# Kernel optimization log

Measured on AMD Instinct MI355X. Metric: run time of the kernel, lower is better.

## Reference

```python
import jax, jax.numpy as jnp
import numpy as np

B, IN, OUT = 131072, 256, 256
BITWIDTH = 7.0


def setup_inputs() -> dict:
    key = jax.random.key(0)
    k1, k2 = jax.random.split(key)
    # simulated int8 activations (integer-valued float32)
    act_in = jax.random.randint(k1, (B, IN), -127, 128).astype(jnp.float32)
    # UniformWeights: xavier_uniform then weight_quant to the int8 grid
    limit = float(np.sqrt(6.0 / (IN + OUT)))
    w = jax.random.uniform(k2, (OUT, IN), minval=-limit, maxval=limit, dtype=jnp.float32)
    w_range = jnp.max(jnp.abs(w))
    weight_exp = (jnp.ceil(jnp.log2(w_range)) - 7.0).astype(jnp.int32)
    weight = jnp.round(w / w_range * 127.0)  # int8-valued float32 [OUT, IN]
    return {"act_in": act_in, "exp_in": jnp.int32(0), "weight": weight, "weight_exp": weight_exp}


def _round_shift(x, shift):
    # RoundShift: floor-div by 2**shift, add floor(|remainder| / 2**(shift-1)), clip to int8
    two_s = jnp.exp2(shift)
    rt = jnp.floor(x / two_s)
    prob = jnp.abs(x - rt * two_s)
    dec = jnp.floor(prob / jnp.exp2(shift - 1.0))
    return jnp.clip(rt + dec, -127.0, 127.0)


def reference(act_in, exp_in, weight, weight_exp):
    # int8 GEMM simulated in fp32 (exact: |acc| < 2^24)
    temp = act_in @ weight.T  # [B, OUT] int32 accumulator values
    # RangeEstimate: full-tensor abs-max -> bitwidth
    r = jnp.max(jnp.abs(temp))
    bw = jnp.where(r > 0, jnp.ceil(jnp.log2(jnp.maximum(r, 1.0))), 0.0)
    shift = bw - BITWIDTH
    pos = shift > 0
    safe_shift = jnp.maximum(shift, 1.0)
    rounded = _round_shift(temp, safe_shift)
    act_out = jnp.where(pos, rounded, temp).astype(jnp.int8)
    exp_sum = jnp.asarray(exp_in, jnp.int32) + jnp.asarray(weight_exp, jnp.int32)
    exp_out = (exp_sum + jnp.where(pos, shift, 0.0).astype(jnp.int32)).astype(jnp.int16)
    return act_out, exp_out
```

## Files before the change

### kernel.cpp

```cpp
#include <hip/hip_runtime.h>
#include <stdint.h>


#define M_ROWS 131072
#define NK 256
#define BM 64
#define BK 64
#define BKP 72

typedef __attribute__((ext_vector_type(8))) short bf16x8;
typedef __attribute__((ext_vector_type(4))) float f32x4;
typedef __attribute__((ext_vector_type(4))) float fv4;
typedef __attribute__((ext_vector_type(4))) int iv4;
typedef __attribute__((ext_vector_type(4))) unsigned int u32x4;
typedef __attribute__((ext_vector_type(4))) unsigned short us4;

__device__ __forceinline__ uint32_t pack_bf16(float a, float b) {
  return (__float_as_uint(a) >> 16) | (__float_as_uint(b) & 0xFFFF0000u);
}

__global__ void wconv(const float* __restrict__ w, unsigned short* __restrict__ wb) {
  const int i = blockIdx.x * 256 + threadIdx.x;
  const fv4 f = ((const fv4*)w)[i];
  us4 o;
  o.x = (unsigned short)(__float_as_uint(f.x) >> 16);
  o.y = (unsigned short)(__float_as_uint(f.y) >> 16);
  o.z = (unsigned short)(__float_as_uint(f.z) >> 16);
  o.w = (unsigned short)(__float_as_uint(f.w) >> 16);
  ((us4*)wb)[i] = o;
}

__device__ __forceinline__ void gemm_tile(
    const float* __restrict__ act, const unsigned short* __restrict__ wgtb,
    short* As, short* Bs, f32x4 acc[4][4])
{
  const int tid  = threadIdx.x;
  const int bm   = blockIdx.x * BM;
  const int lane = tid & 63;
  const int wave = tid >> 6;
  const int lm   = lane & 15;
  const int lk   = lane >> 4;
  const int wn   = wave * 64;

  const int arow = tid >> 3, aks = (tid & 7) * 8;
  const int brow = tid >> 3, bks = (tid & 7) * 8;

  uint32_t apk[2][4];
  u32x4 breg[8];

#pragma unroll
  for (int j = 0; j < 2; ++j) {
    const float* p = act + (size_t)(bm + arow + j * 32) * NK + aks;
    const fv4 f0 = *(const fv4*)p;
    const fv4 f1 = *((const fv4*)p + 1);
    apk[j][0] = pack_bf16(f0.x, f0.y); apk[j][1] = pack_bf16(f0.z, f0.w);
    apk[j][2] = pack_bf16(f1.x, f1.y); apk[j][3] = pack_bf16(f1.z, f1.w);
  }
#pragma unroll
  for (int j = 0; j < 8; ++j)
    breg[j] = *(const u32x4*)(wgtb + (size_t)(brow + j * 32) * NK + bks);

  for (int kt = 0; kt < NK; kt += BK) {
    __syncthreads();
#pragma unroll
    for (int j = 0; j < 2; ++j)
      *(u32x4*)&As[(arow + j * 32) * BKP + aks] = *(const u32x4*)apk[j];
#pragma unroll
    for (int j = 0; j < 8; ++j)
      *(u32x4*)&Bs[(brow + j * 32) * BKP + bks] = breg[j];
    __syncthreads();

    if (kt + BK < NK) {
      const int ktn = kt + BK;
#pragma unroll
      for (int j = 0; j < 2; ++j) {
        const float* p = act + (size_t)(bm + arow + j * 32) * NK + ktn + aks;
        const fv4 f0 = *(const fv4*)p;
        const fv4 f1 = *((const fv4*)p + 1);
        apk[j][0] = pack_bf16(f0.x, f0.y); apk[j][1] = pack_bf16(f0.z, f0.w);
        apk[j][2] = pack_bf16(f1.x, f1.y); apk[j][3] = pack_bf16(f1.z, f1.w);
      }
#pragma unroll
      for (int j = 0; j < 8; ++j)
        breg[j] = *(const u32x4*)(wgtb + (size_t)(brow + j * 32) * NK + ktn + bks);
    }

#pragma unroll
    for (int kk = 0; kk < BK; kk += 32) {
      bf16x8 af[4], bfr[4];
#pragma unroll
      for (int mi = 0; mi < 4; ++mi)
        af[mi] = *(const bf16x8*)&As[(mi * 16 + lm) * BKP + kk + lk * 8];
#pragma unroll
      for (int ni = 0; ni < 4; ++ni)
        bfr[ni] = *(const bf16x8*)&Bs[(wn + ni * 16 + lm) * BKP + kk + lk * 8];
#pragma unroll
      for (int mi = 0; mi < 4; ++mi)
#pragma unroll
        for (int ni = 0; ni < 4; ++ni)
          acc[mi][ni] = __builtin_amdgcn_mfma_f32_16x16x32_bf16(
              af[mi], bfr[ni], acc[mi][ni], 0, 0, 0);
    }
  }
}

__global__ __launch_bounds__(256, 3) void gemm_max(
    const float* __restrict__ act, const unsigned short* __restrict__ wgtb,
    int* __restrict__ gmax)
{
  __shared__ __align__(16) short As[BM * BKP];
  __shared__ __align__(16) short Bs[NK * BKP];
  __shared__ int smax;
  const int tid = threadIdx.x;
  if (tid == 0) smax = 0;

  f32x4 acc[4][4] = {};
  gemm_tile(act, wgtb, As, Bs, acc);

  int imax = 0;
#pragma unroll
  for (int mi = 0; mi < 4; ++mi)
#pragma unroll
    for (int ni = 0; ni < 4; ++ni)
#pragma unroll
      for (int r = 0; r < 4; ++r) {
        const int iv = (int)acc[mi][ni][r];
        const int a = iv < 0 ? -iv : iv;
        imax = a > imax ? a : imax;
      }
#pragma unroll
  for (int off = 32; off; off >>= 1) {
    const int o = __shfl_xor(imax, off, 64);
    imax = o > imax ? o : imax;
  }
  if ((tid & 63) == 0) atomicMax(&smax, imax);
  __syncthreads();
  if (tid == 0) atomicMax(gmax, smax);
}

__global__ __launch_bounds__(256, 3) void gemm_quant(
    const float* __restrict__ act, const unsigned short* __restrict__ wgtb,
    int* __restrict__ out, const int* __restrict__ gmax,
    const int* __restrict__ exp_in, const int* __restrict__ wexp)
{
  __shared__ __align__(16) short As[BM * BKP];
  __shared__ __align__(16) short Bs[NK * BKP];

  const int rmax = *gmax;
  const int bw = (rmax <= 1) ? 0 : (32 - __clz(rmax - 1));
  const int shift = bw - 7;
  const bool pos = shift > 0;
  const int s = shift < 1 ? 1 : shift;

  f32x4 acc[4][4] = {};
  gemm_tile(act, wgtb, As, Bs, acc);

  const int tid  = threadIdx.x;
  const int bm   = blockIdx.x * BM;
  const int lane = tid & 63;
  const int lm   = lane & 15;
  const int lk   = lane >> 4;
  const int wn   = (tid >> 6) * 64;

#pragma unroll
  for (int mi = 0; mi < 4; ++mi)
#pragma unroll
    for (int ni = 0; ni < 4; ++ni)
#pragma unroll
      for (int r = 0; r < 4; ++r) {
        const int ti = (int)acc[mi][ni][r];
        int q;
        if (pos) {
          const int rt = ti >> s;
          const int dec = (ti - (rt << s)) >> (s - 1);
          q = rt + dec;
          q = q > 127 ? 127 : (q < -127 ? -127 : q);
        } else {
          q = (int)(signed char)(ti & 0xFF);
        }
        const int m = bm + mi * 16 + lk * 4 + r;
        const int n = wn + ni * 16 + lm;
        __builtin_nontemporal_store(q, &out[(size_t)m * NK + n]);
      }

  if (blockIdx.x == 0 && tid == 0) {
    const int e = exp_in[0] + wexp[0] + (pos ? shift : 0);
    out[(size_t)M_ROWS * NK] = (int)(short)e;
  }
}

extern "C" void kernel_launch(void* const* d_in, const int* in_sizes, int n_in,
                              void* d_out, int out_size, void* d_ws, size_t ws_size,
                              hipStream_t stream) {
  const float* act   = (const float*)d_in[0];
  const int* exp_in  = (const int*)d_in[1];
  const float* wgt   = (const float*)d_in[2];
  const int* wexp    = (const int*)d_in[3];
  int* gmax          = (int*)d_ws;
  unsigned short* wb = (unsigned short*)((char*)d_ws + 128);

  (void)hipMemsetAsync(d_ws, 0, sizeof(int), stream);
  wconv<<<dim3(64), dim3(256), 0, stream>>>(wgt, wb);
  gemm_max<<<dim3(M_ROWS / BM), dim3(256), 0, stream>>>(act, wb, gmax);
  gemm_quant<<<dim3(M_ROWS / BM), dim3(256), 0, stream>>>(act, wb, (int*)d_out,
                                                          gmax, exp_in, wexp);
}
```

Baseline: 280.2 us.

## Store raw accumulators in first GEMM pass and requantize in place

Instead of running the GEMM twice (once for the global max, once for quantization), the first pass writes int32 accumulators to the output buffer. A lightweight elementwise pass then requantizes them in place. The memset is folded into the weight conversion kernel. This avoids recomputing the GEMM and rereading activations, at the cost of an extra write and read of the 128MB output buffer.

```diff
diff --git a/kernel.cpp b/kernel.cpp
--- a/kernel.cpp
+++ b/kernel.cpp
@@ -19,7 +19,9 @@
   return (__float_as_uint(a) >> 16) | (__float_as_uint(b) & 0xFFFF0000u);
 }
 
-__global__ void wconv(const float* __restrict__ w, unsigned short* __restrict__ wb) {
+__global__ void wconv(const float* __restrict__ w, unsigned short* __restrict__ wb,
+                      int* __restrict__ gmax) {
+  if (blockIdx.x == 0 && threadIdx.x == 0) *gmax = 0;
   const int i = blockIdx.x * 256 + threadIdx.x;
   const fv4 f = ((const fv4*)w)[i];
   us4 o;
@@ -104,9 +106,9 @@
   }
 }
 
-__global__ __launch_bounds__(256, 3) void gemm_max(
+__global__ __launch_bounds__(256, 3) void gemm_maxstore(
     const float* __restrict__ act, const unsigned short* __restrict__ wgtb,
-    int* __restrict__ gmax)
+    int* __restrict__ out, int* __restrict__ gmax)
 {
   __shared__ __align__(16) short As[BM * BKP];
   __shared__ __align__(16) short Bs[NK * BKP];
@@ -117,6 +119,12 @@
   f32x4 acc[4][4] = {};
   gemm_tile(act, wgtb, As, Bs, acc);
 
+  const int bm   = blockIdx.x * BM;
+  const int lane = tid & 63;
+  const int lm   = lane & 15;
+  const int lk   = lane >> 4;
+  const int wn   = (tid >> 6) * 64;
+
   int imax = 0;
 #pragma unroll
   for (int mi = 0; mi < 4; ++mi)
@@ -124,9 +132,12 @@
     for (int ni = 0; ni < 4; ++ni)
 #pragma unroll
       for (int r = 0; r < 4; ++r) {
-        const int iv = (int)acc[mi][ni][r];
-        const int a = iv < 0 ? -iv : iv;
+        const int ti = (int)acc[mi][ni][r];
+        const int a = ti < 0 ? -ti : ti;
         imax = a > imax ? a : imax;
+        const int m = bm + mi * 16 + lk * 4 + r;
+        const int n = wn + ni * 16 + lm;
+        out[(size_t)m * NK + n] = ti;
       }
 #pragma unroll
   for (int off = 32; off; off >>= 1) {
@@ -138,52 +149,40 @@
   if (tid == 0) atomicMax(gmax, smax);
 }
 
-__global__ __launch_bounds__(256, 3) void gemm_quant(
-    const float* __restrict__ act, const unsigned short* __restrict__ wgtb,
+__global__ __launch_bounds__(256) void quant_pass(
     int* __restrict__ out, const int* __restrict__ gmax,
     const int* __restrict__ exp_in, const int* __restrict__ wexp)
 {
-  __shared__ __align__(16) short As[BM * BKP];
-  __shared__ __align__(16) short Bs[NK * BKP];
-
   const int rmax = *gmax;
   const int bw = (rmax <= 1) ? 0 : (32 - __clz(rmax - 1));
   const int shift = bw - 7;
   const bool pos = shift > 0;
   const int s = shift < 1 ? 1 : shift;
 
-  f32x4 acc[4][4] = {};
-  gemm_tile(act, wgtb, As, Bs, acc);
-
-  const int tid  = threadIdx.x;
-  const int bm   = blockIdx.x * BM;
-  const int lane = tid & 63;
-  const int lm   = lane & 15;
-  const int lk   = lane >> 4;
-  const int wn   = (tid >> 6) * 64;
-
-#pragma unroll
-  for (int mi = 0; mi < 4; ++mi)
-#pragma unroll
-    for (int ni = 0; ni < 4; ++ni)
-#pragma unroll
-      for (int r = 0; r < 4; ++r) {
-        const int ti = (int)acc[mi][ni][r];
-        int q;
-        if (pos) {
-          const int rt = ti >> s;
-          const int dec = (ti - (rt << s)) >> (s - 1);
-          q = rt + dec;
-          q = q > 127 ? 127 : (q < -127 ? -127 : q);
-        } else {
-          q = (int)(signed char)(ti & 0xFF);
-        }
-        const int m = bm + mi * 16 + lk * 4 + r;
-        const int n = wn + ni * 16 + lm;
-        __builtin_nontemporal_store(q, &out[(size_t)m * NK + n]);
+  const size_t total  = (size_t)M_ROWS * NK / 4;
+  const size_t stride = (size_t)gridDim.x * blockDim.x;
+  for (size_t i = (size_t)blockIdx.x * blockDim.x + threadIdx.x; i < total;
+       i += stride) {
+    iv4 t = ((const iv4*)out)[i];
+    iv4 q;
+#pragma unroll
+    for (int j = 0; j < 4; ++j) {
+      const int ti = t[j];
+      int r;
+      if (pos) {
+        const int rt = ti >> s;
+        const int dec = (ti - (rt << s)) >> (s - 1);
+        r = rt + dec;
+        r = r > 127 ? 127 : (r < -127 ? -127 : r);
+      } else {
+        r = (int)(signed char)(ti & 0xFF);
       }
-
-  if (blockIdx.x == 0 && tid == 0) {
+      q[j] = r;
+    }
+    __builtin_nontemporal_store(q, &((iv4*)out)[i]);
+  }
+
+  if (blockIdx.x == 0 && threadIdx.x == 0) {
     const int e = exp_in[0] + wexp[0] + (pos ? shift : 0);
     out[(size_t)M_ROWS * NK] = (int)(short)e;
   }
@@ -199,9 +198,8 @@
   int* gmax          = (int*)d_ws;
   unsigned short* wb = (unsigned short*)((char*)d_ws + 128);
 
-  (void)hipMemsetAsync(d_ws, 0, sizeof(int), stream);
-  wconv<<<dim3(64), dim3(256), 0, stream>>>(wgt, wb);
-  gemm_max<<<dim3(M_ROWS / BM), dim3(256), 0, stream>>>(act, wb, gmax);
-  gemm_quant<<<dim3(M_ROWS / BM), dim3(256), 0, stream>>>(act, wb, (int*)d_out,
-                                                          gmax, exp_in, wexp);
-}
+  wconv<<<dim3(64), dim3(256), 0, stream>>>(wgt, wb, gmax);
+  gemm_maxstore<<<dim3(M_ROWS / BM), dim3(256), 0, stream>>>(act, wb, (int*)d_out,
+                                                             gmax);
+  quant_pass<<<dim3(2048), dim3(256), 0, stream>>>((int*)d_out, gmax, exp_in, wexp);
+}
```

New measurement: 280.2 us. About the same (-0.0%).
